# Kernel optimization log

Measured on AMD Instinct MI355X. Metric: run time of the kernel, lower is better.

## Reference

```python
import jax, jax.numpy as jnp
import numpy as np

# Module configuration (from init_kwargs)
N, C_IN, C_OUT, L, V, P = 4, 64, 64, 1024, 25, 3
KERNEL_SIZE, STRIDE = 9, 1
EPS = 1e-5


def _toeplitz(length):
    # Faithful to: sum_i pad(eye(L - stride*i), (i*stride, 0, 0, i*stride))
    # -> ones at [r, r + i*stride] for i in range(kernel_size // stride)
    t = jnp.zeros((length, length), dtype=jnp.float32)
    for i in range(KERNEL_SIZE // STRIDE):  # small fixed loop over taps
        t = t + jnp.eye(length, k=i * STRIDE, dtype=jnp.float32)
    return t


def setup_inputs() -> dict:
    key = jax.random.key(0)
    k0, k1, k2, k3 = jax.random.split(key, 4)
    x = jax.random.normal(k0, (N, C_IN, L, V), dtype=jnp.float32)
    A = jax.random.uniform(k1, (P, V, V), dtype=jnp.float32)
    edge_importance = jnp.ones((P, V, V), dtype=jnp.float32)
    conv_w = jax.random.normal(k2, (C_OUT * P, C_IN, 1, 1), dtype=jnp.float32) * 0.05
    conv_b = jax.random.normal(k3, (C_OUT * P,), dtype=jnp.float32) * 0.05
    gamma = jnp.ones((C_OUT,), dtype=jnp.float32)
    beta = jnp.zeros((C_OUT,), dtype=jnp.float32)
    return {"x": x, "A": A, "edge_importance": edge_importance,
            "conv_w": conv_w, "conv_b": conv_b, "gamma": gamma, "beta": beta}


def reference(x, A, edge_importance, conv_w, conv_b, gamma, beta):
    n, _, l, v = x.shape
    res = x  # residual: in_channels == out_channels and stride == 1 -> identity

    # 1x1 conv: (N, C_in, L, V) -> (N, P*C_out, L, V)
    w = conv_w[:, :, 0, 0]  # (P*C_out, C_in)
    y = jnp.einsum('nclv,kc->nklv', x, w) + conv_b[None, :, None, None]

    # split into P chunks of C_out along channels, stack, permute -> (N, L, P, C_out, V)
    y = y.reshape(n, P, C_OUT, l, v).transpose(0, 3, 1, 2, 4)

    # partition-wise graph adjacency matmul with edge-importance mask
    y = jnp.einsum('nlpcv,pvw->nlpcw', y, A * edge_importance)

    # Toeplitz temporal conv: (N, P, C, V, L) @ (L, L)
    y = y.transpose(0, 2, 3, 4, 1)
    y = jnp.matmul(y, _toeplitz(l))
    y = y.sum(axis=1)            # sum over partitions -> (N, C, V, L)
    y = y.transpose(0, 1, 3, 2)  # (N, C, L, V)

    # BatchNorm2d with batch statistics (track_running_stats=False) + ReLU
    mean = y.mean(axis=(0, 2, 3), keepdims=True)
    var = y.var(axis=(0, 2, 3), keepdims=True)  # biased, as torch uses for normalization
    y = (y - mean) * jax.lax.rsqrt(var + EPS)
    y = y * gamma[None, :, None, None] + beta[None, :, None, None]
    y = jax.nn.relu(y)

    # do = Sequential(ReLU, Dropout(0.0)) applied to (y + res)
    return jax.nn.relu(y + res)
```

## Files before the change

kernel.cpp:

```cpp
#include <hip/hip_runtime.h>
#include <hip/hip_cooperative_groups.h>

namespace cg = cooperative_groups;


typedef unsigned short ushort_t;
typedef __attribute__((ext_vector_type(8))) short short8;
typedef __attribute__((ext_vector_type(4))) float f32x4;
typedef __attribute__((ext_vector_type(4))) unsigned short us4;

#define N_  4
#define CI_ 64
#define CO_ 64
#define L_  1024
#define V_  25
#define P_  3
#define KS_ 9
#define NLV 102400.0f
#define NREP 32
#define TSTR 406

__device__ __forceinline__ float b2f(ushort_t u) {
  union { float f; unsigned int i; } c; c.i = ((unsigned int)u) << 16; return c.f;
}
__device__ __forceinline__ ushort_t f2b(float f) {
  union { float f; unsigned int i; } c; c.f = f;
  unsigned int u = c.i;
  u += 0x7fffu + ((u >> 16) & 1u);
  return (ushort_t)(u >> 16);
}

__global__ __launch_bounds__(256) void kwin(
    const float* __restrict__ x, ushort_t* __restrict__ xs,
    const float* __restrict__ A, const float* __restrict__ E,
    const float* __restrict__ cb, const float* __restrict__ W,
    ushort_t* __restrict__ a2raw, float* __restrict__ biastab,
    ushort_t* __restrict__ wb, float* __restrict__ statsbuf)
{
  const int bx = blockIdx.x;
  const int n = blockIdx.y;
  const int tid = threadIdx.x;

  if (bx == 256) {
    if (n != 0) return;
    __shared__ float colA[P_ * 32];
    if (tid < P_ * 32) {
      int p = tid >> 5, w = tid & 31;
      float s = 0.f;
      if (w < V_)
        for (int v = 0; v < V_; ++v) {
          int idx = (p * V_ + v) * V_ + w;
          s += A[idx] * E[idx];
        }
      colA[tid] = s;
    }
    for (int e = tid; e < 32 * 96; e += 256) {
      int w = e / 96, k = e - w * 96;
      int p = k >> 5, v = k & 31;
      float val = 0.f;
      if (w < V_ && v < V_) {
        int idx = (p * V_ + v) * V_ + w;
        val = A[idx] * E[idx];
      }
      a2raw[e] = f2b(val);
    }
    for (int e = tid; e < 192 * 64; e += 256) wb[e] = f2b(W[e]);
    __syncthreads();
    for (int e = tid; e < 32 * 64; e += 256) {
      int w = e >> 6, c = e & 63;
      float s = 0.f;
      for (int p = 0; p < P_; ++p) s += cb[p * 64 + c] * colA[p * 32 + w];
      biastab[e] = s;
    }
    for (int e = tid; e < NREP * 128; e += 256) statsbuf[e] = 0.f;
    return;
  }

  const int chunk = bx >> 1, half = bx & 1;
  __shared__ __align__(16) ushort_t tile[32 * TSTR];
  const int l0 = chunk * 8;
  const long xn = (long)n * CI_ * L_ * V_ + (long)(half * 32) * (L_ * V_);
  for (int m = tid; m < 3200; m += 256) {
    int ci = m / 100;
    int j4 = (m - ci * 100) * 4;
    f32x4 d;
    if (chunk == 0 && j4 < 200) {
      d = (f32x4){0.f, 0.f, 0.f, 0.f};
    } else {
      d = *(const f32x4*)(x + xn + (long)ci * (L_ * V_) + (l0 - 8) * V_ + j4);
    }
    unsigned int p0 = (unsigned int)f2b(d[0]) | ((unsigned int)f2b(d[1]) << 16);
    unsigned int p1 = (unsigned int)f2b(d[2]) | ((unsigned int)f2b(d[3]) << 16);
    *(unsigned int*)(&tile[ci * TSTR + j4])     = p0;
    *(unsigned int*)(&tile[ci * TSTR + j4 + 2]) = p1;
  }
  __syncthreads();
  const long xsbase = ((long)n * L_ + l0) * 1600 + half * 32;
  for (int cp = tid; cp < 400; cp += 256) {
    const int v = cp >> 4, ci = (cp & 15) * 2;
    const ushort_t* c0 = &tile[ci * TSTR + v];
    const ushort_t* c1 = c0 + TSTR;
    float s0 = 0.f, s1 = 0.f;
#pragma unroll
    for (int li = 0; li < 9; ++li) { s0 += b2f(c0[li * 25]); s1 += b2f(c1[li * 25]); }
    *(unsigned int*)(xs + xsbase + v * 64 + ci) =
        (unsigned int)f2b(s0) | ((unsigned int)f2b(s1) << 16);
#pragma unroll
    for (int l_ = 1; l_ < 8; ++l_) {
      s0 += b2f(c0[(l_ + 8) * 25]) - b2f(c0[(l_ - 1) * 25]);
      s1 += b2f(c1[(l_ + 8) * 25]) - b2f(c1[(l_ - 1) * 25]);
      *(unsigned int*)(xs + xsbase + l_ * 1600 + v * 64 + ci) =
          (unsigned int)f2b(s0) | ((unsigned int)f2b(s1) << 16);
    }
  }
}

template<bool COOP>
__global__ __launch_bounds__(256, 4) void kmain(
    const ushort_t* __restrict__ xs,
    const ushort_t* __restrict__ Wb,
    const ushort_t* __restrict__ a2,
    const float*    __restrict__ biastab,
    ushort_t*       __restrict__ zb,
    float*          __restrict__ statsbuf,
    const float*    __restrict__ gamma,
    const float*    __restrict__ beta,
    const float*    __restrict__ x,
    float*          __restrict__ out)
{
  const int lb = blockIdx.x;
  const int n  = blockIdx.y;
  const int tid = threadIdx.x, lane = tid & 63, wv = tid >> 6;
  const int m16 = lane & 15, quad = lane >> 4;

  __shared__ __align__(16) ushort_t T1[13312];

  short8 af[3][2];
#pragma unroll
  for (int i = 0; i < 3; ++i) {
    const ushort_t* wrow = Wb + ((wv * 3 + i) * 16 + m16) * 64 + quad * 8;
    af[i][0] = *(const short8*)(wrow);
    af[i][1] = *(const short8*)(wrow + 32);
  }

  const ushort_t* xsb = xs + ((long)n * L_ + 4 * lb) * 1600;
  const int cbase = wv * 16 + quad * 4;
  float s1[4] = {0.f, 0.f, 0.f, 0.f}, s2[4] = {0.f, 0.f, 0.f, 0.f};
  us4 zpack[2][2][2];

#pragma unroll
  for (int pair = 0; pair < 2; ++pair) {
    short8 bfr[4][2];
#pragma unroll
    for (int nt = 0; nt < 4; ++nt) {
      const int v = (nt & 1) * 16 + m16;
      const int l_ = pair * 2 + (nt >> 1);
#pragma unroll
      for (int ks = 0; ks < 2; ++ks) {
        short8 t = (short8){0, 0, 0, 0, 0, 0, 0, 0};
        if (v < V_)
          t = *(const short8*)(xsb + l_ * 1600 + v * 64 + ks * 32 + quad * 8);
        bfr[nt][ks] = t;
      }
    }

    f32x4 acc1[3][4];
#pragma unroll
    for (int i = 0; i < 3; ++i)
#pragma unroll
      for (int j = 0; j < 4; ++j) acc1[i][j] = (f32x4){0.f, 0.f, 0.f, 0.f};

#pragma unroll
    for (int i = 0; i < 3; ++i)
#pragma unroll
      for (int nt = 0; nt < 4; ++nt) {
        acc1[i][nt] = __builtin_amdgcn_mfma_f32_16x16x32_bf16(af[i][0], bfr[nt][0], acc1[i][nt], 0, 0, 0);
        acc1[i][nt] = __builtin_amdgcn_mfma_f32_16x16x32_bf16(af[i][1], bfr[nt][1], acc1[i][nt], 0, 0, 0);
      }

    if (pair) __syncthreads();
#pragma unroll
    for (int i = 0; i < 3; ++i) {
      const int mt = wv * 3 + i;
#pragma unroll
      for (int nt = 0; nt < 4; ++nt) {
        const int l_ = nt >> 1;
        const int col = (nt & 1) * 16 + m16;
#pragma unroll
        for (int r = 0; r < 4; ++r) {
          int k = mt * 16 + quad * 4 + r;
          T1[l_ * 6656 + (k & 63) * 104 + (k >> 6) * 32 + col] = f2b(acc1[i][nt][r]);
        }
      }
    }
    __syncthreads();

    short8 bfr2[2][3];
#pragma unroll
    for (int nt = 0; nt < 2; ++nt)
#pragma unroll
      for (int ks = 0; ks < 3; ++ks)
        bfr2[nt][ks] = *(const short8*)(a2 + (nt * 16 + m16) * 96 + ks * 32 + quad * 8);

    f32x4 acc2[2][2];
#pragma unroll
    for (int l_ = 0; l_ < 2; ++l_)
#pragma unroll
      for (int nt = 0; nt < 2; ++nt) acc2[l_][nt] = (f32x4){0.f, 0.f, 0.f, 0.f};

#pragma unroll
    for (int l_ = 0; l_ < 2; ++l_)
#pragma unroll
      for (int ks = 0; ks < 3; ++ks) {
        short8 afT = *(const short8*)(&T1[l_ * 6656 + (wv * 16 + m16) * 104 + ks * 32 + quad * 8]);
        acc2[l_][0] = __builtin_amdgcn_mfma_f32_16x16x32_bf16(afT, bfr2[0][ks], acc2[l_][0], 0, 0, 0);
        acc2[l_][1] = __builtin_amdgcn_mfma_f32_16x16x32_bf16(afT, bfr2[1][ks], acc2[l_][1], 0, 0, 0);
      }

#pragma unroll
    for (int l_ = 0; l_ < 2; ++l_) {
      const int l = 4 * lb + pair * 2 + l_;
      const float cnt = (float)(l + 1 < KS_ ? l + 1 : KS_);
#pragma unroll
      for (int nt = 0; nt < 2; ++nt) {
        const int w = nt * 16 + m16;
        if (w < V_) {
          f32x4 bias = *(const f32x4*)(biastab + w * 64 + cbase);
          us4 pack;
#pragma unroll
          for (int r = 0; r < 4; ++r) {
            pack[r] = f2b(acc2[l_][nt][r] + cnt * bias[r]);
            float zr = b2f(pack[r]);
            s1[r] += zr; s2[r] += zr * zr;
          }
          if constexpr (COOP)
            zpack[pair][l_][nt] = pack;
          else
            *(us4*)(&zb[(((long)(n * L_ + l) * V_ + w) << 6) + cbase]) = pack;
        }
      }
    }
  }
#pragma unroll
  for (int off = 1; off < 16; off <<= 1) {
#pragma unroll
    for (int r = 0; r < 4; ++r) {
      s1[r] += __shfl_xor(s1[r], off, 64);
      s2[r] += __shfl_xor(s2[r], off, 64);
    }
  }
  if (m16 == 0) {
    float* sb = statsbuf + ((n * 256 + lb) & (NREP - 1)) * 128;
#pragma unroll
    for (int r = 0; r < 4; ++r) {
      atomicAdd(&sb[cbase + r], s1[r]);
      atomicAdd(&sb[64 + cbase + r], s2[r]);
    }
  }

  if constexpr (COOP) {
    __syncthreads();
    ushort_t* zl = T1;
#pragma unroll
    for (int pair = 0; pair < 2; ++pair)
#pragma unroll
      for (int l_ = 0; l_ < 2; ++l_)
#pragma unroll
        for (int nt = 0; nt < 2; ++nt) {
          const int w = nt * 16 + m16;
          if (w < V_) {
            const int rr = (pair * 2 + l_) * 25 + w;
            const int e = ((rr >> 2) & 31) << 1;
            const us4 pk = zpack[pair][l_][nt];
            *(unsigned int*)(&zl[rr * 68 + (cbase ^ e)]) =
                (unsigned int)pk[0] | ((unsigned int)pk[1] << 16);
            *(unsigned int*)(&zl[rr * 68 + ((cbase + 2) ^ e)]) =
                (unsigned int)pk[2] | ((unsigned int)pk[3] << 16);
          }
        }

    const long obase = (long)(n * 64) * (L_ * V_) + lb * 100;
    f32x4 xv[7];
#pragma unroll
    for (int i = 0; i < 7; ++i) {
      const int m = tid + i * 256;
      if (m < 1600) {
        const int c = m / 25, q = m - c * 25;
        xv[i] = *(const f32x4*)(x + obase + (long)c * (L_ * V_) + q * 4);
      }
    }

    cg::this_grid().sync();

    float* part = (float*)&T1[8192];
    float* scsh = (float*)&T1[8704];
    {
      const int slot = tid & 127, hf = tid >> 7;
      float a = 0.f;
      for (int k = hf; k < NREP; k += 2)
        a += __hip_atomic_load(&statsbuf[k * 128 + slot],
                               __ATOMIC_RELAXED, __HIP_MEMORY_SCOPE_AGENT);
      part[tid] = a;
    }
    __syncthreads();
    if (tid < 64) {
      const float inv = 1.0f / NLV;
      float s    = part[tid]      + part[128 + tid];
      float sq   = part[64 + tid] + part[192 + tid];
      float mean = s * inv;
      float var  = sq * inv - mean * mean;
      float rstd = rsqrtf(var + 1e-5f);
      float g = gamma[tid];
      scsh[tid]      = rstd * g;
      scsh[64 + tid] = beta[tid] - mean * rstd * g;
    }
    __syncthreads();

#pragma unroll
    for (int i = 0; i < 7; ++i) {
      const int m = tid + i * 256;
      if (m < 1600) {
        const int c = m / 25, q = m - c * 25, rr = q * 4;
        const int e = q << 1;
        const long xi = obase + (long)c * (L_ * V_) + rr;
        const float scc = scsh[c], shc = scsh[64 + c];
        f32x4 o;
#pragma unroll
        for (int j = 0; j < 4; ++j) {
          float z = b2f(zl[(rr + j) * 68 + (c ^ e)]);
          float y = fmaxf(z * scc + shc, 0.f);
          o[j] = fmaxf(y + xv[i][j], 0.f);
        }
        *(f32x4*)(out + xi) = o;
      }
    }
  }
}

__global__ __launch_bounds__(256) void kapply(
    const ushort_t* __restrict__ zb, const float* __restrict__ x,
    const float* __restrict__ statsbuf,
    const float* __restrict__ gamma, const float* __restrict__ beta,
    float* __restrict__ out)
{
  const int n = blockIdx.y, chunk = blockIdx.x;
  const int tid = threadIdx.x;
  __shared__ __align__(16) ushort_t zl[200 * 66];
  __shared__ f32x4 red[8][32];
  __shared__ float sc[64], sh[64];
  const long zbase = (long)((n * L_ + chunk * 8) * V_) * 64;
  for (int m = tid; m < 6400; m += 256) {
    const int row = m >> 5, c2 = (m & 31) * 2;
    const int cs = c2 ^ (((row >> 2) & 31) << 1);
    *(unsigned int*)(&zl[row * 66 + cs]) = ((const unsigned int*)(zb + zbase))[m];
  }
  {
    const int s4 = tid & 31, grp = tid >> 5;
    const f32x4* sb4 = (const f32x4*)statsbuf;
    f32x4 a = (f32x4){0.f, 0.f, 0.f, 0.f};
    for (int k = grp; k < NREP; k += 8) {
      f32x4 v = sb4[k * 32 + s4];
      a[0] += v[0]; a[1] += v[1]; a[2] += v[2]; a[3] += v[3];
    }
    red[grp][s4] = a;
  }
  __syncthreads();
  if (tid < 64) {
    const float inv = 1.0f / NLV;
    float s = 0.f, sq = 0.f;
#pragma unroll
    for (int g = 0; g < 8; ++g) {
      s  += red[g][tid >> 2][tid & 3];
      sq += red[g][16 + (tid >> 2)][tid & 3];
    }
    float mean = s * inv;
    float var  = sq * inv - mean * mean;
    float rstd = rsqrtf(var + 1e-5f);
    float g = gamma[tid];
    sc[tid] = rstd * g;
    sh[tid] = beta[tid] - mean * rstd * g;
  }
  __syncthreads();
  const long obase = ((long)(n * 64) * L_ + chunk * 8) * V_;
  for (int m = tid; m < 3200; m += 256) {
    int c = m / 50, q = m - c * 50, rr = q * 4;
    const int e = ((q & 31) << 1);
    long xi = obase + (long)c * (L_ * V_) + rr;
    f32x4 xv = *(const f32x4*)(x + xi);
    const float scc = sc[c], shc = sh[c];
    f32x4 o;
#pragma unroll
    for (int j = 0; j < 4; ++j) {
      float z = b2f(zl[(rr + j) * 66 + (c ^ e)]);
      float y = fmaxf(z * scc + shc, 0.f);
      o[j] = fmaxf(y + xv[j], 0.f);
    }
    *(f32x4*)(out + xi) = o;
  }
}

extern "C" void kernel_launch(void* const* d_in, const int* in_sizes, int n_in,
                              void* d_out, int out_size, void* d_ws, size_t ws_size,
                              hipStream_t stream)
{
  const float* x     = (const float*)d_in[0];
  const float* A     = (const float*)d_in[1];
  const float* E     = (const float*)d_in[2];
  const float* W     = (const float*)d_in[3];
  const float* cb    = (const float*)d_in[4];
  const float* gamma = (const float*)d_in[5];
  const float* beta  = (const float*)d_in[6];
  float* out = (float*)d_out;

  char* ws = (char*)d_ws;
  const size_t XS_OFF   = 0;
  const size_t ZB_OFF   = 13107200;
  const size_t WB_OFF   = 26214400;
  const size_t A2_OFF   = WB_OFF + 32768;
  const size_t BIAS_OFF = A2_OFF + 16384;
  const size_t STAT_OFF = BIAS_OFF + 16384;
  ushort_t* xs       = (ushort_t*)(ws + XS_OFF);
  ushort_t* zb       = (ushort_t*)(ws + ZB_OFF);
  ushort_t* wb       = (ushort_t*)(ws + WB_OFF);
  ushort_t* a2       = (ushort_t*)(ws + A2_OFF);
  float*    biastab  = (float*)(ws + BIAS_OFF);
  float*    statsbuf = (float*)(ws + STAT_OFF);

  kwin<<<dim3(257, N_), 256, 0, stream>>>(x, xs, A, E, cb, W, a2, biastab, wb,
                                          statsbuf);

  auto kcoop = kmain<true>;
  int maxb = 0;
  hipError_t qe = hipOccupancyMaxActiveBlocksPerMultiprocessor(&maxb, kcoop, 256, 0);
  bool coop = (qe == hipSuccess) && (maxb >= 4);

  if (coop) {
    void* args[] = {&xs, &wb, &a2, &biastab, &zb, &statsbuf,
                    (void*)&gamma, (void*)&beta, (void*)&x, &out};
    hipError_t le = hipLaunchCooperativeKernel((const void*)kcoop,
                                               dim3(256, N_), dim3(256),
                                               args, 0, stream);
    if (le != hipSuccess) coop = false;
  }
  if (!coop) {
    kmain<false><<<dim3(256, N_), 256, 0, stream>>>(
        xs, wb, a2, biastab, zb, statsbuf, gamma, beta, x, out);
    kapply<<<dim3(128, N_), 256, 0, stream>>>(zb, x, statsbuf, gamma, beta, out);
  }
}
```

Baseline: 129.4 us.

## Fuse windowed-input prep kernel into cooperative main kernel behind grid sync

Moves the work of the separate prep kernel (bf16 sliding-window sums of x, weight and adjacency conversion, bias table, stats zeroing) into the prologue of the cooperative main kernel, followed by a grid-wide sync. This removes one kernel launch and its launch gap. The cost is an extra grid barrier, and a few blocks of batch 1 carry extra setup work. The separate prep launch is kept only for the non-cooperative fallback path.

Measured after the change: 130.4 us. Within noise of the previous version (+0.7%).

```diff
diff --git a/kernel.cpp b/kernel.cpp
--- a/kernel.cpp
+++ b/kernel.cpp
@@ -117,15 +117,17 @@
 
 template<bool COOP>
 __global__ __launch_bounds__(256, 4) void kmain(
-    const ushort_t* __restrict__ xs,
-    const ushort_t* __restrict__ Wb,
-    const ushort_t* __restrict__ a2,
-    const float*    __restrict__ biastab,
+    const float*    __restrict__ x,
+    ushort_t*       __restrict__ xs,
+    const float*    __restrict__ A, const float* __restrict__ E,
+    const float*    __restrict__ cb, const float* __restrict__ W,
+    ushort_t*       __restrict__ wb,
+    ushort_t*       __restrict__ a2,
+    float*          __restrict__ biastab,
     ushort_t*       __restrict__ zb,
     float*          __restrict__ statsbuf,
     const float*    __restrict__ gamma,
     const float*    __restrict__ beta,
-    const float*    __restrict__ x,
     float*          __restrict__ out)
 {
   const int lb = blockIdx.x;
@@ -134,11 +136,92 @@
   const int m16 = lane & 15, quad = lane >> 4;
 
   __shared__ __align__(16) ushort_t T1[13312];
+  __shared__ float colA[P_ * 32];
+
+  if constexpr (COOP) {
+    ushort_t* tile = T1;
+    const int chunk = lb >> 1, half = lb & 1;
+    const int l0 = chunk * 8;
+    const long xn = (long)n * CI_ * L_ * V_ + (long)(half * 32) * (L_ * V_);
+    for (int m = tid; m < 3200; m += 256) {
+      int ci = m / 100;
+      int j4 = (m - ci * 100) * 4;
+      f32x4 d;
+      if (chunk == 0 && j4 < 200) {
+        d = (f32x4){0.f, 0.f, 0.f, 0.f};
+      } else {
+        d = *(const f32x4*)(x + xn + (long)ci * (L_ * V_) + (l0 - 8) * V_ + j4);
+      }
+      unsigned int p0 = (unsigned int)f2b(d[0]) | ((unsigned int)f2b(d[1]) << 16);
+      unsigned int p1 = (unsigned int)f2b(d[2]) | ((unsigned int)f2b(d[3]) << 16);
+      *(unsigned int*)(&tile[ci * TSTR + j4])     = p0;
+      *(unsigned int*)(&tile[ci * TSTR + j4 + 2]) = p1;
+    }
+    if (n == 1) {
+      if (lb == 0) {
+        for (int e = tid; e < 32 * 96; e += 256) {
+          int w = e / 96, k = e - w * 96;
+          int p = k >> 5, v = k & 31;
+          float val = 0.f;
+          if (w < V_ && v < V_) {
+            int idx = (p * V_ + v) * V_ + w;
+            val = A[idx] * E[idx];
+          }
+          a2[e] = f2b(val);
+        }
+      } else if (lb == 1) {
+        for (int e = tid; e < 6144; e += 256) wb[e] = f2b(W[e]);
+      } else if (lb == 2) {
+        for (int e = tid; e < 6144; e += 256) wb[6144 + e] = f2b(W[6144 + e]);
+      } else if (lb == 3) {
+        for (int e = tid; e < NREP * 128; e += 256) statsbuf[e] = 0.f;
+      } else if (lb == 4) {
+        if (tid < P_ * 32) {
+          int p = tid >> 5, w = tid & 31;
+          float s = 0.f;
+          if (w < V_)
+            for (int v = 0; v < V_; ++v) {
+              int idx = (p * V_ + v) * V_ + w;
+              s += A[idx] * E[idx];
+            }
+          colA[tid] = s;
+        }
+      }
+    }
+    __syncthreads();
+    const long xsbase = ((long)n * L_ + l0) * 1600 + half * 32;
+    for (int cp = tid; cp < 400; cp += 256) {
+      const int v = cp >> 4, ci = (cp & 15) * 2;
+      const ushort_t* c0 = &tile[ci * TSTR + v];
+      const ushort_t* c1 = c0 + TSTR;
+      float s0 = 0.f, s1 = 0.f;
+#pragma unroll
+      for (int li = 0; li < 9; ++li) { s0 += b2f(c0[li * 25]); s1 += b2f(c1[li * 25]); }
+      *(unsigned int*)(xs + xsbase + v * 64 + ci) =
+          (unsigned int)f2b(s0) | ((unsigned int)f2b(s1) << 16);
+#pragma unroll
+      for (int l_ = 1; l_ < 8; ++l_) {
+        s0 += b2f(c0[(l_ + 8) * 25]) - b2f(c0[(l_ - 1) * 25]);
+        s1 += b2f(c1[(l_ + 8) * 25]) - b2f(c1[(l_ - 1) * 25]);
+        *(unsigned int*)(xs + xsbase + l_ * 1600 + v * 64 + ci) =
+            (unsigned int)f2b(s0) | ((unsigned int)f2b(s1) << 16);
+      }
+    }
+    if (n == 1 && lb == 4) {
+      for (int e = tid; e < 32 * 64; e += 256) {
+        int w = e >> 6, c = e & 63;
+        float s = 0.f;
+        for (int p = 0; p < P_; ++p) s += cb[p * 64 + c] * colA[p * 32 + w];
+        biastab[e] = s;
+      }
+    }
+    cg::this_grid().sync();
+  }
 
   short8 af[3][2];
 #pragma unroll
   for (int i = 0; i < 3; ++i) {
-    const ushort_t* wrow = Wb + ((wv * 3 + i) * 16 + m16) * 64 + quad * 8;
+    const ushort_t* wrow = wb + ((wv * 3 + i) * 16 + m16) * 64 + quad * 8;
     af[i][0] = *(const short8*)(wrow);
     af[i][1] = *(const short8*)(wrow + 32);
   }
@@ -178,7 +261,7 @@
         acc1[i][nt] = __builtin_amdgcn_mfma_f32_16x16x32_bf16(af[i][1], bfr[nt][1], acc1[i][nt], 0, 0, 0);
       }
 
-    if (pair) __syncthreads();
+    __syncthreads();
 #pragma unroll
     for (int i = 0; i < 3; ++i) {
       const int mt = wv * 3 + i;
@@ -426,25 +509,25 @@
   float*    biastab  = (float*)(ws + BIAS_OFF);
   float*    statsbuf = (float*)(ws + STAT_OFF);
 
-  kwin<<<dim3(257, N_), 256, 0, stream>>>(x, xs, A, E, cb, W, a2, biastab, wb,
-                                          statsbuf);
-
   auto kcoop = kmain<true>;
   int maxb = 0;
   hipError_t qe = hipOccupancyMaxActiveBlocksPerMultiprocessor(&maxb, kcoop, 256, 0);
   bool coop = (qe == hipSuccess) && (maxb >= 4);
 
   if (coop) {
-    void* args[] = {&xs, &wb, &a2, &biastab, &zb, &statsbuf,
-                    (void*)&gamma, (void*)&beta, (void*)&x, &out};
+    void* args[] = {(void*)&x, &xs, (void*)&A, (void*)&E, (void*)&cb, (void*)&W,
+                    &wb, &a2, &biastab, &zb, &statsbuf,
+                    (void*)&gamma, (void*)&beta, &out};
     hipError_t le = hipLaunchCooperativeKernel((const void*)kcoop,
                                                dim3(256, N_), dim3(256),
                                                args, 0, stream);
     if (le != hipSuccess) coop = false;
   }
   if (!coop) {
+    kwin<<<dim3(257, N_), 256, 0, stream>>>(x, xs, A, E, cb, W, a2, biastab, wb,
+                                            statsbuf);
     kmain<false><<<dim3(256, N_), 256, 0, stream>>>(
-        xs, wb, a2, biastab, zb, statsbuf, gamma, beta, x, out);
+        x, xs, A, E, cb, W, wb, a2, biastab, zb, statsbuf, gamma, beta, out);
     kapply<<<dim3(128, N_), 256, 0, stream>>>(zb, x, statsbuf, gamma, beta, out);
   }
 }
```
